# Performance work log

Measured on AMD Instinct MI355X. Metric: run time of the kernel, lower is better.

## Reference

```python
import jax, jax.numpy as jnp
import numpy as np

NF = 64
G_OFF = 4          # offset groups
K = 9              # 3x3 kernel taps


def lrelu(x):
    return jnp.where(x >= 0, x, 0.1 * x)


def conv3(x, w, b):
    # 3x3 conv, stride 1, pad 1, NCHW / OIHW
    y = jax.lax.conv_general_dilated(
        x, w, window_strides=(1, 1), padding=((1, 1), (1, 1)),
        dimension_numbers=('NCHW', 'OIHW', 'NCHW'))
    return y + b[None, :, None, None]


def deform_conv2d(x, offset, w, b, g_off):
    # torchvision-style DCNv1: 3x3, stride 1, pad 1, weight groups = 1
    B, C, H, W = x.shape
    Cg = C // g_off
    O = w.shape[0]
    # offset layout: [B, 2*g*K, H, W] -> [B, g, K, (dy,dx), H, W]
    off = offset.reshape(B, g_off, K, 2, H, W)
    ky = jnp.repeat(jnp.arange(3), 3).astype(x.dtype)  # kernel row per tap
    kx = jnp.tile(jnp.arange(3), 3).astype(x.dtype)    # kernel col per tap
    py = jnp.arange(H, dtype=x.dtype)[None, :, None] - 1.0 + ky[:, None, None]  # [K,H,1]
    px = jnp.arange(W, dtype=x.dtype)[None, None, :] - 1.0 + kx[:, None, None]  # [K,1,W]
    sy = off[:, :, :, 0] + py[None, None]  # [B,g,K,H,W] sampling rows
    sx = off[:, :, :, 1] + px[None, None]  # [B,g,K,H,W] sampling cols
    y0 = jnp.floor(sy)
    x0 = jnp.floor(sx)
    feat = x.reshape(B, g_off, Cg, H * W)
    acc = jnp.zeros((B, g_off, Cg, K * H * W), dtype=x.dtype)
    for dyc, dxc in ((0.0, 0.0), (0.0, 1.0), (1.0, 0.0), (1.0, 1.0)):
        yc = y0 + dyc
        xc = x0 + dxc
        wgt = (1.0 - jnp.abs(sy - yc)) * (1.0 - jnp.abs(sx - xc))
        valid = (yc >= 0) & (yc < H) & (xc >= 0) & (xc < W)
        wgt = jnp.where(valid, wgt, 0.0)
        idx = (jnp.clip(yc, 0, H - 1).astype(jnp.int32) * W
               + jnp.clip(xc, 0, W - 1).astype(jnp.int32))
        gathered = jnp.take_along_axis(feat, idx.reshape(B, g_off, 1, K * H * W), axis=3)
        acc = acc + gathered * wgt.reshape(B, g_off, 1, K * H * W)
    sampled = acc.reshape(B, C, K, H, W)
    out = jnp.einsum('bckhw,ock->bohw', sampled, w.reshape(O, C, K))
    return out + b[None, :, None, None]


def setup_inputs() -> dict:
    key = jax.random.key(0)
    ks = jax.random.split(key, 16)
    B, H, W = 4, 128, 224
    off_ch = 2 * G_OFF * 9  # 72
    s = 0.05
    inp = {
        'nbr_fea_l': jax.random.normal(ks[0], (B, NF, H, W), jnp.float32),
        'ref_fea_l': jax.random.normal(ks[1], (B, NF, H, W), jnp.float32),
        'w_co1': jax.random.normal(ks[2], (NF, 2 * NF, 3, 3), jnp.float32) * s,
        'b_co1': jnp.zeros((NF,), jnp.float32),
        'w_m1': jax.random.normal(ks[3], (NF, NF, 3, 3), jnp.float32) * s,
        'b_m1': jnp.zeros((NF,), jnp.float32),
        'w_m2': jax.random.normal(ks[4], (NF, NF, 3, 3), jnp.float32) * s,
        'b_m2': jnp.zeros((NF,), jnp.float32),
        'w_m3': jax.random.normal(ks[5], (off_ch, NF, 3, 3), jnp.float32) * 0.01,
        'b_m3': jnp.zeros((off_ch,), jnp.float32),
        'w_dcn': jax.random.normal(ks[6], (NF, NF, 3, 3), jnp.float32) * s,
        'b_dcn': jnp.zeros((NF,), jnp.float32),
    }
    return inp


def reference(nbr_fea_l, ref_fea_l, w_co1, b_co1, w_m1, b_m1, w_m2, b_m2,
              w_m3, b_m3, w_dcn, b_dcn):
    feat = lrelu(conv3(jnp.concatenate([nbr_fea_l, ref_fea_l], axis=1), w_co1, b_co1))
    # MotionNet offset head (assumed 3-layer conv stack)
    off = lrelu(conv3(feat, w_m1, b_m1))
    off = lrelu(conv3(off, w_m2, b_m2))
    off = conv3(off, w_m3, b_m3)  # [B, 2*G*9, H, W]
    return lrelu(deform_conv2d(nbr_fea_l, off, w_dcn, b_dcn, G_OFF))
```

## Files before the change

kernel.cpp:

```cpp
#include <hip/hip_runtime.h>

#define HH 128
#define WW 224
#define HW_ (HH * WW)

typedef short short8 __attribute__((ext_vector_type(8)));
typedef float f32x4 __attribute__((ext_vector_type(4)));
typedef float float2v __attribute__((ext_vector_type(2)));

__device__ __forceinline__ float lrelu_f(float v) { return v >= 0.f ? v : 0.1f * v; }

__device__ __forceinline__ unsigned short f2bf(float f) {
  union { float f; unsigned u; } x; x.f = f;
  unsigned r = x.u + 0x7fff + ((x.u >> 16) & 1);
  return (unsigned short)(r >> 16);
}
__device__ __forceinline__ float bf2f(unsigned short u) {
  union { unsigned u; float f; } x; x.u = ((unsigned)u) << 16; return x.f;
}
__device__ __forceinline__ float asf(unsigned u) {
  union { unsigned u; float f; } x; x.u = u; return x.f;
}

__device__ __forceinline__ void wfrag_one(const float* __restrict__ w,
                                          unsigned short* __restrict__ wt,
                                          int i, int O, int C, int NFT) {
  const int CB = C / 32;
  const int j = i & 7;
  const int lane = (i >> 3) & 63;
  const int fid = i >> 9;
  const int nfg = fid % NFT;
  const int kcb = fid / NFT;
  const int cb = kcb % CB;
  const int k = kcb / CB;
  const int o = nfg * 16 + (lane & 15);
  const int c = cb * 32 + (lane >> 4) * 8 + j;
  float v = (o < O) ? w[((size_t)o * C + c) * 9 + k] : 0.f;
  wt[i] = f2bf(v);
}
__device__ __forceinline__ void wdcn_one(const float* __restrict__ w,
                                         unsigned short* __restrict__ wt, int i) {
  const int j = i & 7;
  const int lane = (i >> 3) & 63;
  const int fid = i >> 9;
  const int mf = fid & 3;
  const int s = (fid >> 2) % 5;
  const int g = fid / 20;
  const int l15 = lane & 15, lg = lane >> 4;
  const int o = mf * 16 + l15;
  const int t = 2 * s + (lg >> 1);
  const int c = g * 16 + (lg & 1) * 8 + j;
  float v = (t < 9) ? w[((size_t)o * 64 + c) * 9 + t] : 0.f;
  wt[i] = f2bf(v);
}

__global__ __launch_bounds__(256)
void prep_all(const float* __restrict__ nbr, const float* __restrict__ ref,
              const float* __restrict__ w1, const float* __restrict__ wm1,
              const float* __restrict__ wm2, const float* __restrict__ wm3,
              const float* __restrict__ wdcn,
              unsigned short* __restrict__ xt, unsigned short* __restrict__ xnb,
              unsigned short* __restrict__ wf1, unsigned short* __restrict__ wfm1,
              unsigned short* __restrict__ wfm2, unsigned short* __restrict__ wfm3,
              unsigned short* __restrict__ wdf) {
  __shared__ __align__(16) char ls[64 * 256];
  if (blockIdx.x >= 1792) {
    int i = (blockIdx.x - 1792) * 256 + threadIdx.x;
    if (i < 73728) { wfrag_one(w1, wf1, i, 64, 128, 4); return; }
    i -= 73728;
    if (i < 36864) { wfrag_one(wm1, wfm1, i, 64, 64, 4); return; }
    i -= 36864;
    if (i < 36864) { wfrag_one(wm2, wfm2, i, 64, 64, 4); return; }
    i -= 36864;
    if (i < 46080) { wfrag_one(wm3, wfm3, i, 72, 64, 5); return; }
    i -= 46080;
    if (i < 40960) wdcn_one(wdcn, wdf, i);
    return;
  }
  const int lane = threadIdx.x & 63;
  const int q = threadIdx.x >> 6;
  const int bxp = blockIdx.x % 448;
  const int b = blockIdx.x / 448;
  const int p0 = bxp * 64;
  const int p = p0 + lane;
  const int c0 = q * 32;
  const float* src = (c0 < 64) ? (nbr + ((size_t)b * 64 + c0) * HW_)
                               : (ref + ((size_t)b * 64 + (c0 - 64)) * HW_);
  unsigned short tmp[32];
  #pragma unroll
  for (int i = 0; i < 32; ++i) tmp[i] = f2bf(src[(size_t)i * HW_ + p]);
  #pragma unroll
  for (int j = 0; j < 4; ++j) {
    const int byte = (c0 * 2 + j * 16) ^ ((lane & 7) << 4);
    *(short8*)(ls + lane * 256 + byte) = *(const short8*)(tmp + j * 8);
  }
  __syncthreads();
  const int tid = threadIdx.x;
  unsigned short* dst = xt + ((size_t)b * HW_ + p0) * 128;
  #pragma unroll
  for (int j = 0; j < 4; ++j) {
    const int unit = tid * 4 + j;
    const int px = unit >> 4, ck = unit & 15;
    const short8 v = *(const short8*)(ls + px * 256 + ((ck * 16) ^ ((px & 7) << 4)));
    *(short8*)(dst + (size_t)px * 128 + ck * 8) = v;
  }
  unsigned short* dst2 = xnb + ((size_t)b * HW_ + p0) * 64;
  #pragma unroll
  for (int j = 0; j < 2; ++j) {
    const int unit = tid * 2 + j;
    const int px = unit >> 3, ck = unit & 7;
    const short8 v = *(const short8*)(ls + px * 256 + ((ck * 16) ^ ((px & 7) << 4)));
    *(short8*)(dst2 + (size_t)px * 64 + ck * 8) = v;
  }
}

template<int CINB, int NFT, int CROW, bool LRELU>
__global__ __launch_bounds__(256, 2)
void conv_lds2(const unsigned short* __restrict__ xt, const unsigned short* __restrict__ wfrag,
               const float* __restrict__ bias, unsigned short* __restrict__ out, int coutReal) {
  __shared__ __align__(16) char xs[10 * 34 * 128];
  const int tid = threadIdx.x;
  const int lane = tid & 63, wv = tid >> 6;
  const int l15 = lane & 15, lg = lane >> 4;
  const int b = blockIdx.y;
  const int ty = (blockIdx.x / 7) * 8, tx = (blockIdx.x % 7) * 32;
  const int CIN = CINB * 64;
  const unsigned short* xb = xt + (size_t)b * HW_ * CIN;

  f32x4 acc[4][NFT];
  #pragma unroll
  for (int mf = 0; mf < 4; ++mf)
    #pragma unroll
    for (int nf = 0; nf < NFT; ++nf) acc[mf][nf] = (f32x4){0.f, 0.f, 0.f, 0.f};

  #pragma unroll 1
  for (int cb2 = 0; cb2 < CINB; ++cb2) {
    if (cb2 > 0) __syncthreads();
    for (int ci = tid; ci < 2720; ci += 256) {
      const int ch = ci & 7;
      const int hp = ci >> 3;
      const int hr = hp / 34, hc = hp % 34;
      const int gy = ty + hr - 1, gx = tx + hc - 1;
      short8 v = (short8)0;
      if (((unsigned)gy < HH) & ((unsigned)gx < WW))
        v = *(const short8*)(xb + (size_t)(gy * WW + gx) * CIN + cb2 * 64 + ch * 8);
      *(short8*)(xs + hp * 128 + ((ch * 16) ^ ((hc & 7) << 4))) = v;
    }
    __syncthreads();

    #pragma unroll
    for (int k = 0; k < 9; ++k) {
      const int ky = k / 3, kx = k % 3;
      #pragma unroll
      for (int cb = 0; cb < 2; ++cb) {
        short8 av[4];
        #pragma unroll
        for (int mf = 0; mf < 4; ++mf) {
          const int hr = 2 * wv + (mf >> 1) + ky;
          const int hc = (mf & 1) * 16 + l15 + kx;
          av[mf] = *(const short8*)(xs + (hr * 34 + hc) * 128
                                    + ((cb * 64 + lg * 16) ^ ((hc & 7) << 4)));
        }
        #pragma unroll
        for (int nf = 0; nf < NFT; ++nf) {
          const short8 bv = *(const short8*)(wfrag
              + ((size_t)((k * (CINB * 2) + cb2 * 2 + cb) * NFT + nf)) * 512 + lane * 8);
          #pragma unroll
          for (int mf = 0; mf < 4; ++mf)
            acc[mf][nf] = __builtin_amdgcn_mfma_f32_16x16x32_bf16(av[mf], bv, acc[mf][nf], 0, 0, 0);
        }
      }
    }
  }

  unsigned short* ob = out + (size_t)b * HW_ * CROW;
  #pragma unroll
  for (int nf = 0; nf < NFT; ++nf) {
    const int o = nf * 16 + l15;
    const bool ov = (o < coutReal);
    const float bz = ov ? bias[o] : 0.f;
    #pragma unroll
    for (int mf = 0; mf < 4; ++mf) {
      const int rr = ty + 2 * wv + (mf >> 1);
      #pragma unroll
      for (int r = 0; r < 4; ++r) {
        const int cc = tx + (mf & 1) * 16 + lg * 4 + r;
        float vv = acc[mf][nf][r] + bz;
        if (LRELU) vv = lrelu_f(vv);
        if (ov) ob[(size_t)(rr * WW + cc) * CROW + o] = f2bf(vv);
      }
    }
  }
}

template<int CINB, int NFT, int CROW, bool LRELU>
__global__ __launch_bounds__(256, 2)
void conv_lds(const unsigned short* __restrict__ xt, const unsigned short* __restrict__ wfrag,
              const float* __restrict__ bias, unsigned short* __restrict__ out, int coutReal) {
  __shared__ __align__(16) char xs[6 * 34 * 128];
  const int tid = threadIdx.x;
  const int lane = tid & 63, wv = tid >> 6;
  const int l15 = lane & 15, lg = lane >> 4;
  const int b = blockIdx.y;
  const int ty = (blockIdx.x / 7) * 4, tx = (blockIdx.x % 7) * 32;
  const int CIN = CINB * 64;
  const unsigned short* xb = xt + (size_t)b * HW_ * CIN;

  f32x4 acc[2][NFT];
  #pragma unroll
  for (int mf = 0; mf < 2; ++mf)
    #pragma unroll
    for (int nf = 0; nf < NFT; ++nf) acc[mf][nf] = (f32x4){0.f, 0.f, 0.f, 0.f};

  #pragma unroll 1
  for (int cb2 = 0; cb2 < CINB; ++cb2) {
    if (cb2 > 0) __syncthreads();
    for (int ci = tid; ci < 1632; ci += 256) {
      const int ch = ci & 7;
      const int hp = ci >> 3;
      const int hr = hp / 34, hc = hp % 34;
      const int gy = ty + hr - 1, gx = tx + hc - 1;
      short8 v = (short8)0;
      if (((unsigned)gy < HH) & ((unsigned)gx < WW))
        v = *(const short8*)(xb + (size_t)(gy * WW + gx) * CIN + cb2 * 64 + ch * 8);
      *(short8*)(xs + hp * 128 + ((ch * 16) ^ ((hc & 7) << 4))) = v;
    }
    __syncthreads();

    #pragma unroll
    for (int k = 0; k < 9; ++k) {
      const int ky = k / 3, kx = k % 3;
      #pragma unroll
      for (int cb = 0; cb < 2; ++cb) {
        short8 av[2];
        #pragma unroll
        for (int mf = 0; mf < 2; ++mf) {
          const int hr = wv + ky;
          const int hc = mf * 16 + l15 + kx;
          av[mf] = *(const short8*)(xs + (hr * 34 + hc) * 128
                                    + ((cb * 64 + lg * 16) ^ ((hc & 7) << 4)));
        }
        #pragma unroll
        for (int nf = 0; nf < NFT; ++nf) {
          const short8 bv = *(const short8*)(wfrag
              + ((size_t)((k * (CINB * 2) + cb2 * 2 + cb) * NFT + nf)) * 512 + lane * 8);
          #pragma unroll
          for (int mf = 0; mf < 2; ++mf)
            acc[mf][nf] = __builtin_amdgcn_mfma_f32_16x16x32_bf16(av[mf], bv, acc[mf][nf], 0, 0, 0);
        }
      }
    }
  }

  unsigned short* ob = out + (size_t)b * HW_ * CROW;
  const int rr = ty + wv;
  #pragma unroll
  for (int nf = 0; nf < NFT; ++nf) {
    const int o = nf * 16 + l15;
    const bool ov = (o < coutReal);
    const float bz = ov ? bias[o] : 0.f;
    #pragma unroll
    for (int mf = 0; mf < 2; ++mf) {
      #pragma unroll
      for (int r = 0; r < 4; ++r) {
        const int cc = tx + mf * 16 + lg * 4 + r;
        float vv = acc[mf][nf][r] + bz;
        if (LRELU) vv = lrelu_f(vv);
        if (ov) ob[(size_t)(rr * WW + cc) * CROW + o] = f2bf(vv);
      }
    }
  }
}

__global__ __launch_bounds__(256, 2)
void dcn_v8(const unsigned short* __restrict__ xnb,
            const unsigned short* __restrict__ offt,
            const unsigned short* __restrict__ wdf,
            const float* __restrict__ bias, float* __restrict__ out) {
  __shared__ __align__(16) char xs[10 * 20 * 128];
  const int tid = threadIdx.x;
  const int w = tid >> 6, l = tid & 63;
  const int l15 = l & 15, lg = l >> 4;
  const int b = blockIdx.y;
  const int bx = blockIdx.x;
  const int swz = (bx & 7) * 56 + (bx >> 3);
  const int tx = (swz % 14) * 16;
  const int ty = (swz / 14) * 4;
  const int y = ty + w;
  const int x = tx + l15;
  const int p_img = y * WW + x;
  const unsigned short* xb = xnb + (size_t)b * HW_ * 64;

  for (int ci = tid; ci < 1600; ci += 256) {
    const int ch = ci & 7;
    const int pos = ci >> 3;
    const int r = pos / 20, c = pos % 20;
    const int gy = ty - 3 + r, gx = tx - 2 + c;
    short8 v = (short8)0;
    if (((unsigned)gy < HH) & ((unsigned)gx < WW))
      v = *(const short8*)(xb + (size_t)(gy * WW + gx) * 64 + ch * 8);
    *(short8*)(xs + pos * 128 + ((ch * 16) ^ (((r + c) & 7) << 4))) = v;
  }
  __syncthreads();

  const unsigned* od = (const unsigned*)(offt + ((size_t)b * HW_ + p_img) * 72);
  const int thalf = lg >> 1;
  const int cofs0 = (lg & 1) * 8;

  float pyA[5], pxA[5];
  int liveA[5];
  #pragma unroll
  for (int s = 0; s < 5; ++s) {
    const int t = 2 * s + thalf;
    liveA[s] = (t < 9);
    const int tt = liveA[s] ? t : 0;
    pyA[s] = (float)(y - 1 + tt / 3);
    pxA[s] = (float)(x - 1 + tt % 3);
  }

  f32x4 acc[4];
  #pragma unroll
  for (int mf = 0; mf < 4; ++mf) acc[mf] = (f32x4){0.f, 0.f, 0.f, 0.f};

  #pragma unroll 1
  for (int g = 0; g < 4; ++g) {
    const int cofs = g * 16 + cofs0;
    const int chunkB = cofs * 2;
    #pragma unroll
    for (int s = 0; s < 5; ++s) {
      const int live = liveA[s];
      const int t = 2 * s + thalf;
      const unsigned dpair = od[g * 9 + (live ? t : 0)];
      const float dy = bf2f((unsigned short)(dpair & 0xffff));
      const float dx = bf2f((unsigned short)(dpair >> 16));
      const float sy = dy + pyA[s];
      const float sx = dx + pxA[s];
      const float fy = floorf(sy);
      const float fx = floorf(sx);
      const int y0 = (int)fy;
      const int x0 = (int)fx;
      const float ay = sy - fy;
      const float ax = sx - fx;
      const float by = 1.f - ay, bxx = 1.f - ax;
      float w00 = by * bxx, w01 = by * ax, w10 = ay * bxx, w11 = ay * ax;
      const int ry0 = y0 - ty + 3;
      const int rx0 = x0 - tx + 2;
      const bool inT = (!live) | (((unsigned)ry0 < 9u) & ((unsigned)rx0 < 19u));
      short8 q00, q01, q10, q11;
      if (__all((int)inT)) {
        const int r0 = live ? ry0 : 0;
        const int c0 = live ? rx0 : 0;
        const int b00 = (r0 * 20 + c0) << 7;
        const int sw00 = b00 + (chunkB ^ (((r0 + c0) & 7) << 4));
        const int sw01 = b00 + 128 + (chunkB ^ (((r0 + c0 + 1) & 7) << 4));
        const int b10 = b00 + 2560;
        const int sw10 = b10 + (chunkB ^ (((r0 + c0 + 1) & 7) << 4));
        const int sw11 = b10 + 128 + (chunkB ^ (((r0 + c0 + 2) & 7) << 4));
        q00 = *(const short8*)(xs + sw00);
        q01 = *(const short8*)(xs + sw01);
        q10 = *(const short8*)(xs + sw10);
        q11 = *(const short8*)(xs + sw11);
      } else {
        const bool vy0 = (y0 >= 0) & (y0 < HH);
        const bool vy1 = (y0 + 1 >= 0) & (y0 + 1 < HH);
        const bool vx0 = (x0 >= 0) & (x0 < WW);
        const bool vx1 = (x0 + 1 >= 0) & (x0 + 1 < WW);
        w00 = (vy0 & vx0) ? w00 : 0.f;
        w01 = (vy0 & vx1) ? w01 : 0.f;
        w10 = (vy1 & vx0) ? w10 : 0.f;
        w11 = (vy1 & vx1) ? w11 : 0.f;
        const int cy0 = min(max(y0, 0), HH - 1);
        const int cy1 = min(max(y0 + 1, 0), HH - 1);
        const int cx0 = min(max(x0, 0), WW - 1);
        const int cx1 = min(max(x0 + 1, 0), WW - 1);
        q00 = *(const short8*)(xb + (size_t)(cy0 * WW + cx0) * 64 + cofs);
        q01 = *(const short8*)(xb + (size_t)(cy0 * WW + cx1) * 64 + cofs);
        q10 = *(const short8*)(xb + (size_t)(cy1 * WW + cx0) * 64 + cofs);
        q11 = *(const short8*)(xb + (size_t)(cy1 * WW + cx1) * 64 + cofs);
      }
      short8 pf = (short8)0;
      if (live) {
        const unsigned* u00 = (const unsigned*)&q00;
        const unsigned* u01 = (const unsigned*)&q01;
        const unsigned* u10 = (const unsigned*)&q10;
        const unsigned* u11 = (const unsigned*)&q11;
        unsigned pr[4];
        #pragma unroll
        for (int i = 0; i < 4; ++i) {
          float2v f00, f01, f10, f11;
          f00.x = asf(u00[i] << 16); f00.y = asf(u00[i] & 0xffff0000u);
          f01.x = asf(u01[i] << 16); f01.y = asf(u01[i] & 0xffff0000u);
          f10.x = asf(u10[i] << 16); f10.y = asf(u10[i] & 0xffff0000u);
          f11.x = asf(u11[i] << 16); f11.y = asf(u11[i] & 0xffff0000u);
          const float2v s2 = f00 * w00 + f01 * w01 + f10 * w10 + f11 * w11;
          unsigned pk;
          asm("v_cvt_pk_bf16_f32 %0, %1, %2" : "=v"(pk) : "v"(s2.x), "v"(s2.y));
          pr[i] = pk;
        }
        pf = *(const short8*)pr;
      }
      #pragma unroll
      for (int mf = 0; mf < 4; ++mf) {
        const short8 wf = *(const short8*)(wdf + ((size_t)((g * 5 + s) * 4 + mf)) * 512 + l * 8);
        acc[mf] = __builtin_amdgcn_mfma_f32_16x16x32_bf16(wf, pf, acc[mf], 0, 0, 0);
      }
    }
  }

  float* ob = out + (size_t)b * 64 * HW_;
  #pragma unroll
  for (int mf = 0; mf < 4; ++mf) {
    #pragma unroll
    for (int r = 0; r < 4; ++r) {
      const int o = mf * 16 + lg * 4 + r;
      ob[(size_t)o * HW_ + p_img] = lrelu_f(acc[mf][r] + bias[o]);
    }
  }
}

extern "C" void kernel_launch(void* const* d_in, const int* in_sizes, int n_in,
                              void* d_out, int out_size, void* d_ws, size_t ws_size,
                              hipStream_t stream) {
  const float* nbr   = (const float*)d_in[0];
  const float* ref   = (const float*)d_in[1];
  const float* w_co1 = (const float*)d_in[2];
  const float* b_co1 = (const float*)d_in[3];
  const float* w_m1  = (const float*)d_in[4];
  const float* b_m1  = (const float*)d_in[5];
  const float* w_m2  = (const float*)d_in[6];
  const float* b_m2  = (const float*)d_in[7];
  const float* w_m3  = (const float*)d_in[8];
  const float* b_m3  = (const float*)d_in[9];
  const float* w_dcn = (const float*)d_in[10];
  const float* b_dcn = (const float*)d_in[11];
  float* out = (float*)d_out;

  char* ws = (char*)d_ws;
  unsigned short* xnb   = (unsigned short*)(ws);
  unsigned short* x1t   = (unsigned short*)(ws + 14680064);
  unsigned short* m1t   = (unsigned short*)(ws + 14680064);
  unsigned short* m2t   = (unsigned short*)(ws + 29360128);
  unsigned short* featt = (unsigned short*)(ws + 44040192);
  unsigned short* offt  = (unsigned short*)(ws + 44040192);
  char* wbase = ws + 60555264;
  unsigned short* wf1  = (unsigned short*)(wbase);
  unsigned short* wfm1 = (unsigned short*)(wbase + 147456);
  unsigned short* wfm2 = (unsigned short*)(wbase + 221184);
  unsigned short* wfm3 = (unsigned short*)(wbase + 294912);
  unsigned short* wdf  = (unsigned short*)(wbase + 387072);

  dim3 blk(256);
  prep_all<<<dim3(2708), blk, 0, stream>>>(nbr, ref, w_co1, w_m1, w_m2, w_m3, w_dcn,
                                           x1t, xnb, wf1, wfm1, wfm2, wfm3, wdf);

  conv_lds2<2, 4, 64, true ><<<dim3(112, 4), blk, 0, stream>>>(x1t,   wf1,  b_co1, featt, 64);
  conv_lds2<1, 4, 64, true ><<<dim3(112, 4), blk, 0, stream>>>(featt, wfm1, b_m1,  m1t,   64);
  conv_lds2<1, 4, 64, true ><<<dim3(112, 4), blk, 0, stream>>>(m1t,   wfm2, b_m2,  m2t,   64);
  conv_lds <1, 5, 72, false><<<dim3(224, 4), blk, 0, stream>>>(m2t,   wfm3, b_m3,  offt,  72);
  dcn_v8<<<dim3(448, 4), blk, 0, stream>>>(xnb, offt, wdf, b_dcn, out);
}
```

Before: 165.6 us.

## Fuse offset conv into deformable conv kernel and drop concatenated input copy

The final 3x3 offset convolution (64->72 channels) now runs inside the deformable-conv kernel. Each block stages a halo of the m2 activations in LDS, computes offsets with MFMA split across waves by kernel tap, and reduces them into an fp32 LDS buffer with atomics. This removes one launch and the round trip of the offset tensor through global memory, and keeps the offsets in fp32 instead of bf16. The prep kernel also stops writing a separate 128-channel concatenated copy, and the first conv reads nbr and ref from two buffers. The cost is much more LDS per block, possibly lower occupancy, recomputed offset-conv halos, and LDS atomic contention.

```diff
diff --git a/kernel.cpp b/kernel.cpp
--- a/kernel.cpp
+++ b/kernel.cpp
@@ -59,7 +59,7 @@
               const float* __restrict__ w1, const float* __restrict__ wm1,
               const float* __restrict__ wm2, const float* __restrict__ wm3,
               const float* __restrict__ wdcn,
-              unsigned short* __restrict__ xt, unsigned short* __restrict__ xnb,
+              unsigned short* __restrict__ xnb, unsigned short* __restrict__ xref,
               unsigned short* __restrict__ wf1, unsigned short* __restrict__ wfm1,
               unsigned short* __restrict__ wfm2, unsigned short* __restrict__ wfm3,
               unsigned short* __restrict__ wdf) {
@@ -96,27 +96,28 @@
   }
   __syncthreads();
   const int tid = threadIdx.x;
-  unsigned short* dst = xt + ((size_t)b * HW_ + p0) * 128;
-  #pragma unroll
-  for (int j = 0; j < 4; ++j) {
-    const int unit = tid * 4 + j;
-    const int px = unit >> 4, ck = unit & 15;
-    const short8 v = *(const short8*)(ls + px * 256 + ((ck * 16) ^ ((px & 7) << 4)));
-    *(short8*)(dst + (size_t)px * 128 + ck * 8) = v;
-  }
-  unsigned short* dst2 = xnb + ((size_t)b * HW_ + p0) * 64;
+  unsigned short* dnb = xnb + ((size_t)b * HW_ + p0) * 64;
+  unsigned short* drf = xref + ((size_t)b * HW_ + p0) * 64;
   #pragma unroll
   for (int j = 0; j < 2; ++j) {
     const int unit = tid * 2 + j;
     const int px = unit >> 3, ck = unit & 7;
     const short8 v = *(const short8*)(ls + px * 256 + ((ck * 16) ^ ((px & 7) << 4)));
-    *(short8*)(dst2 + (size_t)px * 64 + ck * 8) = v;
+    *(short8*)(dnb + (size_t)px * 64 + ck * 8) = v;
+  }
+  #pragma unroll
+  for (int j = 0; j < 2; ++j) {
+    const int unit = tid * 2 + j;
+    const int px = unit >> 3, ck = unit & 7;
+    const short8 v = *(const short8*)(ls + px * 256 + (((ck + 8) * 16) ^ ((px & 7) << 4)));
+    *(short8*)(drf + (size_t)px * 64 + ck * 8) = v;
   }
 }
 
 template<int CINB, int NFT, int CROW, bool LRELU>
 __global__ __launch_bounds__(256, 2)
-void conv_lds2(const unsigned short* __restrict__ xt, const unsigned short* __restrict__ wfrag,
+void conv_lds2(const unsigned short* __restrict__ x0, const unsigned short* __restrict__ x1,
+               const unsigned short* __restrict__ wfrag,
                const float* __restrict__ bias, unsigned short* __restrict__ out, int coutReal) {
   __shared__ __align__(16) char xs[10 * 34 * 128];
   const int tid = threadIdx.x;
@@ -124,8 +125,6 @@
   const int l15 = lane & 15, lg = lane >> 4;
   const int b = blockIdx.y;
   const int ty = (blockIdx.x / 7) * 8, tx = (blockIdx.x % 7) * 32;
-  const int CIN = CINB * 64;
-  const unsigned short* xb = xt + (size_t)b * HW_ * CIN;
 
   f32x4 acc[4][NFT];
   #pragma unroll
@@ -136,6 +135,7 @@
   #pragma unroll 1
   for (int cb2 = 0; cb2 < CINB; ++cb2) {
     if (cb2 > 0) __syncthreads();
+    const unsigned short* xb = (cb2 ? x1 : x0) + (size_t)b * HW_ * 64;
     for (int ci = tid; ci < 2720; ci += 256) {
       const int ch = ci & 7;
       const int hp = ci >> 3;
@@ -143,7 +143,7 @@
       const int gy = ty + hr - 1, gx = tx + hc - 1;
       short8 v = (short8)0;
       if (((unsigned)gy < HH) & ((unsigned)gx < WW))
-        v = *(const short8*)(xb + (size_t)(gy * WW + gx) * CIN + cb2 * 64 + ch * 8);
+        v = *(const short8*)(xb + (size_t)(gy * WW + gx) * 64 + ch * 8);
       *(short8*)(xs + hp * 128 + ((ch * 16) ^ ((hc & 7) << 4))) = v;
     }
     __syncthreads();
@@ -193,91 +193,16 @@
   }
 }
 
-template<int CINB, int NFT, int CROW, bool LRELU>
 __global__ __launch_bounds__(256, 2)
-void conv_lds(const unsigned short* __restrict__ xt, const unsigned short* __restrict__ wfrag,
-              const float* __restrict__ bias, unsigned short* __restrict__ out, int coutReal) {
-  __shared__ __align__(16) char xs[6 * 34 * 128];
-  const int tid = threadIdx.x;
-  const int lane = tid & 63, wv = tid >> 6;
-  const int l15 = lane & 15, lg = lane >> 4;
-  const int b = blockIdx.y;
-  const int ty = (blockIdx.x / 7) * 4, tx = (blockIdx.x % 7) * 32;
-  const int CIN = CINB * 64;
-  const unsigned short* xb = xt + (size_t)b * HW_ * CIN;
-
-  f32x4 acc[2][NFT];
-  #pragma unroll
-  for (int mf = 0; mf < 2; ++mf)
-    #pragma unroll
-    for (int nf = 0; nf < NFT; ++nf) acc[mf][nf] = (f32x4){0.f, 0.f, 0.f, 0.f};
-
-  #pragma unroll 1
-  for (int cb2 = 0; cb2 < CINB; ++cb2) {
-    if (cb2 > 0) __syncthreads();
-    for (int ci = tid; ci < 1632; ci += 256) {
-      const int ch = ci & 7;
-      const int hp = ci >> 3;
-      const int hr = hp / 34, hc = hp % 34;
-      const int gy = ty + hr - 1, gx = tx + hc - 1;
-      short8 v = (short8)0;
-      if (((unsigned)gy < HH) & ((unsigned)gx < WW))
-        v = *(const short8*)(xb + (size_t)(gy * WW + gx) * CIN + cb2 * 64 + ch * 8);
-      *(short8*)(xs + hp * 128 + ((ch * 16) ^ ((hc & 7) << 4))) = v;
-    }
-    __syncthreads();
-
-    #pragma unroll
-    for (int k = 0; k < 9; ++k) {
-      const int ky = k / 3, kx = k % 3;
-      #pragma unroll
-      for (int cb = 0; cb < 2; ++cb) {
-        short8 av[2];
-        #pragma unroll
-        for (int mf = 0; mf < 2; ++mf) {
-          const int hr = wv + ky;
-          const int hc = mf * 16 + l15 + kx;
-          av[mf] = *(const short8*)(xs + (hr * 34 + hc) * 128
-                                    + ((cb * 64 + lg * 16) ^ ((hc & 7) << 4)));
-        }
-        #pragma unroll
-        for (int nf = 0; nf < NFT; ++nf) {
-          const short8 bv = *(const short8*)(wfrag
-              + ((size_t)((k * (CINB * 2) + cb2 * 2 + cb) * NFT + nf)) * 512 + lane * 8);
-          #pragma unroll
-          for (int mf = 0; mf < 2; ++mf)
-            acc[mf][nf] = __builtin_amdgcn_mfma_f32_16x16x32_bf16(av[mf], bv, acc[mf][nf], 0, 0, 0);
-        }
-      }
-    }
-  }
-
-  unsigned short* ob = out + (size_t)b * HW_ * CROW;
-  const int rr = ty + wv;
-  #pragma unroll
-  for (int nf = 0; nf < NFT; ++nf) {
-    const int o = nf * 16 + l15;
-    const bool ov = (o < coutReal);
-    const float bz = ov ? bias[o] : 0.f;
-    #pragma unroll
-    for (int mf = 0; mf < 2; ++mf) {
-      #pragma unroll
-      for (int r = 0; r < 4; ++r) {
-        const int cc = tx + mf * 16 + lg * 4 + r;
-        float vv = acc[mf][nf][r] + bz;
-        if (LRELU) vv = lrelu_f(vv);
-        if (ov) ob[(size_t)(rr * WW + cc) * CROW + o] = f2bf(vv);
-      }
-    }
-  }
-}
-
-__global__ __launch_bounds__(256, 2)
-void dcn_v8(const unsigned short* __restrict__ xnb,
-            const unsigned short* __restrict__ offt,
+void dcn_v9(const unsigned short* __restrict__ xnb,
+            const unsigned short* __restrict__ m2t,
+            const unsigned short* __restrict__ wfm3,
+            const float* __restrict__ bm3,
             const unsigned short* __restrict__ wdf,
             const float* __restrict__ bias, float* __restrict__ out) {
   __shared__ __align__(16) char xs[10 * 20 * 128];
+  __shared__ __align__(16) char m2s[6 * 18 * 128];
+  __shared__ __align__(16) float odl[64 * 82];
   const int tid = threadIdx.x;
   const int w = tid >> 6, l = tid & 63;
   const int l15 = l & 15, lg = l >> 4;
@@ -290,7 +215,18 @@
   const int x = tx + l15;
   const int p_img = y * WW + x;
   const unsigned short* xb = xnb + (size_t)b * HW_ * 64;
-
+  const unsigned short* m2b = m2t + (size_t)b * HW_ * 64;
+
+  for (int ci = tid; ci < 864; ci += 256) {
+    const int ch = ci & 7;
+    const int pos = ci >> 3;
+    const int r = pos / 18, c = pos % 18;
+    const int gy = ty - 1 + r, gx = tx - 1 + c;
+    short8 v = (short8)0;
+    if (((unsigned)gy < HH) & ((unsigned)gx < WW))
+      v = *(const short8*)(m2b + (size_t)(gy * WW + gx) * 64 + ch * 8);
+    *(short8*)(m2s + pos * 128 + ((ch * 16) ^ ((c & 7) << 4))) = v;
+  }
   for (int ci = tid; ci < 1600; ci += 256) {
     const int ch = ci & 7;
     const int pos = ci >> 3;
@@ -301,9 +237,58 @@
       v = *(const short8*)(xb + (size_t)(gy * WW + gx) * 64 + ch * 8);
     *(short8*)(xs + pos * 128 + ((ch * 16) ^ (((r + c) & 7) << 4))) = v;
   }
+  for (int u = tid; u < 5120; u += 256) {
+    const int o = u % 80;
+    odl[(u / 80) * 82 + o] = (o < 72) ? bm3[o] : 0.f;
+  }
   __syncthreads();
 
-  const unsigned* od = (const unsigned*)(offt + ((size_t)b * HW_ + p_img) * 72);
+  {
+    const int ks = (w == 0) ? 0 : (w == 1) ? 3 : (w == 2) ? 5 : 7;
+    const int ke = (w == 0) ? 3 : (w == 1) ? 5 : (w == 2) ? 7 : 9;
+    f32x4 acc3[4][5];
+    #pragma unroll
+    for (int rf = 0; rf < 4; ++rf)
+      #pragma unroll
+      for (int nf = 0; nf < 5; ++nf) acc3[rf][nf] = (f32x4){0.f, 0.f, 0.f, 0.f};
+    #pragma unroll 1
+    for (int k = ks; k < ke; ++k) {
+      const int ky = k / 3, kx = k % 3;
+      #pragma unroll
+      for (int cb = 0; cb < 2; ++cb) {
+        short8 av[4];
+        #pragma unroll
+        for (int rf = 0; rf < 4; ++rf) {
+          const int hc = l15 + kx;
+          av[rf] = *(const short8*)(m2s + ((rf + ky) * 18 + hc) * 128
+                                    + ((cb * 64 + lg * 16) ^ ((hc & 7) << 4)));
+        }
+        #pragma unroll
+        for (int nf = 0; nf < 5; ++nf) {
+          const short8 bv = *(const short8*)(wfm3
+              + ((size_t)((k * 2 + cb) * 5 + nf)) * 512 + l * 8);
+          #pragma unroll
+          for (int rf = 0; rf < 4; ++rf)
+            acc3[rf][nf] = __builtin_amdgcn_mfma_f32_16x16x32_bf16(av[rf], bv, acc3[rf][nf], 0, 0, 0);
+        }
+      }
+    }
+    #pragma unroll
+    for (int rf = 0; rf < 4; ++rf) {
+      #pragma unroll
+      for (int nf = 0; nf < 5; ++nf) {
+        const int o = nf * 16 + l15;
+        #pragma unroll
+        for (int r = 0; r < 4; ++r) {
+          const int px = rf * 16 + lg * 4 + r;
+          atomicAdd(&odl[px * 82 + o], acc3[rf][nf][r]);
+        }
+      }
+    }
+  }
+  __syncthreads();
+
+  const float* myod = odl + (w * 16 + l15) * 82;
   const int thalf = lg >> 1;
   const int cofs0 = (lg & 1) * 8;
 
@@ -330,9 +315,10 @@
     for (int s = 0; s < 5; ++s) {
       const int live = liveA[s];
       const int t = 2 * s + thalf;
-      const unsigned dpair = od[g * 9 + (live ? t : 0)];
-      const float dy = bf2f((unsigned short)(dpair & 0xffff));
-      const float dx = bf2f((unsigned short)(dpair >> 16));
+      const int m = g * 9 + (live ? t : 0);
+      const float2v dp = *(const float2v*)(myod + 2 * m);
+      const float dy = dp.x;
+      const float dx = dp.y;
       const float sy = dy + pyA[s];
       const float sx = dx + pxA[s];
       const float fy = floorf(sy);
@@ -437,12 +423,11 @@
 
   char* ws = (char*)d_ws;
   unsigned short* xnb   = (unsigned short*)(ws);
-  unsigned short* x1t   = (unsigned short*)(ws + 14680064);
-  unsigned short* m1t   = (unsigned short*)(ws + 14680064);
+  unsigned short* xref  = (unsigned short*)(ws + 14680064);
+  unsigned short* featt = (unsigned short*)(ws + 29360128);
+  unsigned short* m1t   = (unsigned short*)(ws + 44040192);
   unsigned short* m2t   = (unsigned short*)(ws + 29360128);
-  unsigned short* featt = (unsigned short*)(ws + 44040192);
-  unsigned short* offt  = (unsigned short*)(ws + 44040192);
-  char* wbase = ws + 60555264;
+  char* wbase = ws + 58720256;
   unsigned short* wf1  = (unsigned short*)(wbase);
   unsigned short* wfm1 = (unsigned short*)(wbase + 147456);
   unsigned short* wfm2 = (unsigned short*)(wbase + 221184);
@@ -451,11 +436,10 @@
 
   dim3 blk(256);
   prep_all<<<dim3(2708), blk, 0, stream>>>(nbr, ref, w_co1, w_m1, w_m2, w_m3, w_dcn,
-                                           x1t, xnb, wf1, wfm1, wfm2, wfm3, wdf);
-
-  conv_lds2<2, 4, 64, true ><<<dim3(112, 4), blk, 0, stream>>>(x1t,   wf1,  b_co1, featt, 64);
-  conv_lds2<1, 4, 64, true ><<<dim3(112, 4), blk, 0, stream>>>(featt, wfm1, b_m1,  m1t,   64);
-  conv_lds2<1, 4, 64, true ><<<dim3(112, 4), blk, 0, stream>>>(m1t,   wfm2, b_m2,  m2t,   64);
-  conv_lds <1, 5, 72, false><<<dim3(224, 4), blk, 0, stream>>>(m2t,   wfm3, b_m3,  offt,  72);
-  dcn_v8<<<dim3(448, 4), blk, 0, stream>>>(xnb, offt, wdf, b_dcn, out);
-}
+                                           xnb, xref, wf1, wfm1, wfm2, wfm3, wdf);
+
+  conv_lds2<2, 4, 64, true ><<<dim3(112, 4), blk, 0, stream>>>(xnb,   xref,  wf1,  b_co1, featt, 64);
+  conv_lds2<1, 4, 64, true ><<<dim3(112, 4), blk, 0, stream>>>(featt, featt, wfm1, b_m1,  m1t,   64);
+  conv_lds2<1, 4, 64, true ><<<dim3(112, 4), blk, 0, stream>>>(m1t,   m1t,   wfm2, b_m2,  m2t,   64);
+  dcn_v9<<<dim3(448, 4), blk, 0, stream>>>(xnb, m2t, wfm3, b_m3, wdf, b_dcn, out);
+}
```

Result: slower. 337.5 us (+103.8%).
